# Kernel tuning notes

Hardware: AMD Instinct MI355X
Metric: run time of the kernel (lower is better)

Reference implementation:

```python
import jax, jax.numpy as jnp
import numpy as np

B = 4096          # number of graphs/segments
D = 256           # n_feature
O = 4             # n_output


def setup_inputs() -> dict:
    key = jax.random.key(0)
    k1, k2 = jax.random.split(key)
    # ragged segment sizes in [32, 96], concrete at trace time
    rng = np.random.default_rng(0)
    counts = rng.integers(32, 97, size=B).astype(np.int64)
    total = int(counts.sum())  # ~262144 nodes
    x = jax.random.normal(k1, (total, D), dtype=jnp.float32)
    W = jax.random.normal(k2, (O, D), dtype=jnp.float32) * (1.0 / np.sqrt(D))
    b = jnp.zeros((O,), dtype=jnp.float32)
    node_num = jnp.asarray(counts)
    return {"x": x, "node_num": node_num, "W": W, "b": b}


def reference(x, node_num, W, b):
    # x: [total_nodes, D]; node_num: [B] contiguous segment sizes
    total = x.shape[0]
    seg_ids = jnp.repeat(jnp.arange(B), node_num, total_repeat_length=total)
    seg_sum = jax.ops.segment_sum(x, seg_ids, num_segments=B)          # [B, D]
    mean = seg_sum / node_num[:, None].astype(x.dtype)                 # per-segment mean
    return jax.nn.sigmoid(mean @ W.T + b)                              # [B, O]
```

## Files before the change

kernel.cpp:

```cpp
#include <hip/hip_runtime.h>
#include <math.h>

#define SCAN_DIM 256

typedef float v4f __attribute__((ext_vector_type(4)));

__global__ void seg_offsets_kernel(const int* __restrict__ counts,
                                   int* __restrict__ offsets, int B) {
  __shared__ int partial[SCAN_DIM];
  const int tid = threadIdx.x;
  const int chunk = (B + SCAN_DIM - 1) / SCAN_DIM;
  const int base = tid * chunk;

  int s = 0;
  for (int i = 0; i < chunk; ++i) {
    const int idx = base + i;
    if (idx < B) s += counts[idx];
  }
  partial[tid] = s;
  __syncthreads();

  for (int off = 1; off < SCAN_DIM; off <<= 1) {
    int v = (tid >= off) ? partial[tid - off] : 0;
    __syncthreads();
    partial[tid] += v;
    __syncthreads();
  }

  int run = (tid == 0) ? 0 : partial[tid - 1];
  for (int i = 0; i < chunk; ++i) {
    const int idx = base + i;
    if (idx < B) {
      offsets[idx] = run;
      run += counts[idx];
    }
  }
}

__global__ __launch_bounds__(64) void mean_proj_kernel(
    const float* __restrict__ x, const int* __restrict__ counts,
    const int* __restrict__ offsets, const float* __restrict__ W,
    const float* __restrict__ b, float* __restrict__ out) {
  const int seg  = blockIdx.x;
  const int lane = threadIdx.x;

  const int  cnt   = counts[seg];
  const long start = (long)offsets[seg];

  const v4f* W4 = (const v4f*)W;
  const v4f w0 = W4[0 * 64 + lane];
  const v4f w1 = W4[1 * 64 + lane];
  const v4f w2 = W4[2 * 64 + lane];
  const v4f w3 = W4[3 * 64 + lane];

  float a0 = 0.f, a1 = 0.f, a2 = 0.f, a3 = 0.f;

  const v4f* p = (const v4f*)x + start * 64 + lane;

  int n = 0;
  v4f v0, v1, v2, v3;
  bool have = (3 < cnt);
  if (have) {
    v0 = __builtin_nontemporal_load(p + 0);
    v1 = __builtin_nontemporal_load(p + 64);
    v2 = __builtin_nontemporal_load(p + 128);
    v3 = __builtin_nontemporal_load(p + 192);
  }
  while (have) {
    const int nn = n + 4;
    const bool next = (nn + 3 < cnt);
    const v4f* q = p + 256;
    v4f u0, u1, u2, u3;
    if (next) {
      u0 = __builtin_nontemporal_load(q + 0);
      u1 = __builtin_nontemporal_load(q + 64);
      u2 = __builtin_nontemporal_load(q + 128);
      u3 = __builtin_nontemporal_load(q + 192);
    }

    a0 += v0.x * w0.x + v0.y * w0.y + v0.z * w0.z + v0.w * w0.w;
    a1 += v0.x * w1.x + v0.y * w1.y + v0.z * w1.z + v0.w * w1.w;
    a2 += v0.x * w2.x + v0.y * w2.y + v0.z * w2.z + v0.w * w2.w;
    a3 += v0.x * w3.x + v0.y * w3.y + v0.z * w3.z + v0.w * w3.w;

    a0 += v1.x * w0.x + v1.y * w0.y + v1.z * w0.z + v1.w * w0.w;
    a1 += v1.x * w1.x + v1.y * w1.y + v1.z * w1.z + v1.w * w1.w;
    a2 += v1.x * w2.x + v1.y * w2.y + v1.z * w2.z + v1.w * w2.w;
    a3 += v1.x * w3.x + v1.y * w3.y + v1.z * w3.z + v1.w * w3.w;

    a0 += v2.x * w0.x + v2.y * w0.y + v2.z * w0.z + v2.w * w0.w;
    a1 += v2.x * w1.x + v2.y * w1.y + v2.z * w1.z + v2.w * w1.w;
    a2 += v2.x * w2.x + v2.y * w2.y + v2.z * w2.z + v2.w * w2.w;
    a3 += v2.x * w3.x + v2.y * w3.y + v2.z * w3.z + v2.w * w3.w;

    a0 += v3.x * w0.x + v3.y * w0.y + v3.z * w0.z + v3.w * w0.w;
    a1 += v3.x * w1.x + v3.y * w1.y + v3.z * w1.z + v3.w * w1.w;
    a2 += v3.x * w2.x + v3.y * w2.y + v3.z * w2.z + v3.w * w2.w;
    a3 += v3.x * w3.x + v3.y * w3.y + v3.z * w3.z + v3.w * w3.w;

    if (next) { v0 = u0; v1 = u1; v2 = u2; v3 = u3; }
    p = q; n = nn; have = next;
  }
  {
    const v4f* t = (const v4f*)x + start * 64 + lane;
    for (; n < cnt; ++n) {
      const v4f v = __builtin_nontemporal_load(t + (long)n * 64);
      a0 += v.x * w0.x + v.y * w0.y + v.z * w0.z + v.w * w0.w;
      a1 += v.x * w1.x + v.y * w1.y + v.z * w1.z + v.w * w1.w;
      a2 += v.x * w2.x + v.y * w2.y + v.z * w2.z + v.w * w2.w;
      a3 += v.x * w3.x + v.y * w3.y + v.z * w3.z + v.w * w3.w;
    }
  }

  for (int off = 32; off > 0; off >>= 1) {
    a0 += __shfl_down(a0, off, 64);
    a1 += __shfl_down(a1, off, 64);
    a2 += __shfl_down(a2, off, 64);
    a3 += __shfl_down(a3, off, 64);
  }

  if (lane == 0) {
    const float inv = 1.0f / (float)cnt;
    v4f r;
    r.x = 1.0f / (1.0f + expf(-(a0 * inv + b[0])));
    r.y = 1.0f / (1.0f + expf(-(a1 * inv + b[1])));
    r.z = 1.0f / (1.0f + expf(-(a2 * inv + b[2])));
    r.w = 1.0f / (1.0f + expf(-(a3 * inv + b[3])));
    *(v4f*)(out + (long)seg * 4) = r;
  }
}

extern "C" void kernel_launch(void* const* d_in, const int* in_sizes, int n_in,
                              void* d_out, int out_size, void* d_ws, size_t ws_size,
                              hipStream_t stream) {
  const float* x        = (const float*)d_in[0];
  const int*   node_num = (const int*)d_in[1];
  const float* W        = (const float*)d_in[2];
  const float* b        = (const float*)d_in[3];
  float*       out      = (float*)d_out;

  const int B = in_sizes[1];
  int* offsets = (int*)d_ws;

  seg_offsets_kernel<<<1, SCAN_DIM, 0, stream>>>(node_num, offsets, B);
  mean_proj_kernel<<<B, 64, 0, stream>>>(x, node_num, offsets, W, b, out);
}
```

Measured before the change: 346.2 us.

## Balance work by splitting rows evenly across waves with atomic segment accumulation

Replaces one-wave-per-segment with a fixed grid of waves that each own an equal chunk of rows, locate their starting segment by binary search over offsets, and flush partial projections to a zeroed accumulator with atomics at segment boundaries. A third kernel then applies the mean scaling, bias and sigmoid. This targets load imbalance from ragged segment sizes and the short per-segment loops. In exchange it adds an extra launch, atomic traffic, per-row boundary checks, and a float summation order that is no longer deterministic.

```diff
diff --git a/kernel.cpp b/kernel.cpp
--- a/kernel.cpp
+++ b/kernel.cpp
@@ -2,11 +2,13 @@
 #include <math.h>
 
 #define SCAN_DIM 256
+#define NWAVES   4096
 
 typedef float v4f __attribute__((ext_vector_type(4)));
 
 __global__ void seg_offsets_kernel(const int* __restrict__ counts,
-                                   int* __restrict__ offsets, int B) {
+                                   int* __restrict__ offsets,
+                                   float* __restrict__ seg_acc, int B) {
   __shared__ int partial[SCAN_DIM];
   const int tid = threadIdx.x;
   const int chunk = (B + SCAN_DIM - 1) / SCAN_DIM;
@@ -35,17 +37,20 @@
       run += counts[idx];
     }
   }
+  if (tid == SCAN_DIM - 1) offsets[B] = run;
+
+  for (int i = tid; i < B * 4; i += SCAN_DIM) seg_acc[i] = 0.0f;
 }
 
-__global__ __launch_bounds__(64) void mean_proj_kernel(
-    const float* __restrict__ x, const int* __restrict__ counts,
-    const int* __restrict__ offsets, const float* __restrict__ W,
-    const float* __restrict__ b, float* __restrict__ out) {
-  const int seg  = blockIdx.x;
+__global__ __launch_bounds__(64) void proj_acc_kernel(
+    const float* __restrict__ x, const int* __restrict__ offsets,
+    const float* __restrict__ W, float* __restrict__ seg_acc,
+    int B, int T, int chunk) {
+  const int wave = blockIdx.x;
   const int lane = threadIdx.x;
-
-  const int  cnt   = counts[seg];
-  const long start = (long)offsets[seg];
+  const int r0 = wave * chunk;
+  if (r0 >= T) return;
+  const int r1 = min(r0 + chunk, T);
 
   const v4f* W4 = (const v4f*)W;
   const v4f w0 = W4[0 * 64 + lane];
@@ -53,13 +58,48 @@
   const v4f w2 = W4[2 * 64 + lane];
   const v4f w3 = W4[3 * 64 + lane];
 
+  int lo = 0, hi = B;
+  while (hi - lo > 1) {
+    const int mid = (lo + hi) >> 1;
+    if (offsets[mid] <= r0) lo = mid; else hi = mid;
+  }
+  int seg    = lo;
+  int segEnd = offsets[seg + 1];
+
   float a0 = 0.f, a1 = 0.f, a2 = 0.f, a3 = 0.f;
 
-  const v4f* p = (const v4f*)x + start * 64 + lane;
+  auto flush = [&]() {
+    float t0 = a0, t1 = a1, t2 = a2, t3 = a3;
+    for (int off = 32; off > 0; off >>= 1) {
+      t0 += __shfl_down(t0, off, 64);
+      t1 += __shfl_down(t1, off, 64);
+      t2 += __shfl_down(t2, off, 64);
+      t3 += __shfl_down(t3, off, 64);
+    }
+    if (lane == 0) {
+      atomicAdd(&seg_acc[seg * 4 + 0], t0);
+      atomicAdd(&seg_acc[seg * 4 + 1], t1);
+      atomicAdd(&seg_acc[seg * 4 + 2], t2);
+      atomicAdd(&seg_acc[seg * 4 + 3], t3);
+    }
+    a0 = a1 = a2 = a3 = 0.f;
+  };
 
-  int n = 0;
+#define ACC(v)                                                      \
+  a0 += (v).x * w0.x + (v).y * w0.y + (v).z * w0.z + (v).w * w0.w;  \
+  a1 += (v).x * w1.x + (v).y * w1.y + (v).z * w1.z + (v).w * w1.w;  \
+  a2 += (v).x * w2.x + (v).y * w2.y + (v).z * w2.z + (v).w * w2.w;  \
+  a3 += (v).x * w3.x + (v).y * w3.y + (v).z * w3.z + (v).w * w3.w;
+
+#define BOUNDARY(r)                                                 \
+  if ((r) == segEnd) { flush(); ++seg; segEnd = offsets[seg + 1]; }
+
+  const v4f* xb = (const v4f*)x + (long)r0 * 64 + lane;
+  const v4f* p  = xb;
+
+  int n = r0;
   v4f v0, v1, v2, v3;
-  bool have = (3 < cnt);
+  bool have = (n + 3 < r1);
   if (have) {
     v0 = __builtin_nontemporal_load(p + 0);
     v1 = __builtin_nontemporal_load(p + 64);
@@ -67,9 +107,9 @@
     v3 = __builtin_nontemporal_load(p + 192);
   }
   while (have) {
-    const int nn = n + 4;
-    const bool next = (nn + 3 < cnt);
-    const v4f* q = p + 256;
+    const int  nn   = n + 4;
+    const bool next = (nn + 3 < r1);
+    const v4f* q    = p + 256;
     v4f u0, u1, u2, u3;
     if (next) {
       u0 = __builtin_nontemporal_load(q + 0);
@@ -78,56 +118,39 @@
       u3 = __builtin_nontemporal_load(q + 192);
     }
 
-    a0 += v0.x * w0.x + v0.y * w0.y + v0.z * w0.z + v0.w * w0.w;
-    a1 += v0.x * w1.x + v0.y * w1.y + v0.z * w1.z + v0.w * w1.w;
-    a2 += v0.x * w2.x + v0.y * w2.y + v0.z * w2.z + v0.w * w2.w;
-    a3 += v0.x * w3.x + v0.y * w3.y + v0.z * w3.z + v0.w * w3.w;
-
-    a0 += v1.x * w0.x + v1.y * w0.y + v1.z * w0.z + v1.w * w0.w;
-    a1 += v1.x * w1.x + v1.y * w1.y + v1.z * w1.z + v1.w * w1.w;
-    a2 += v1.x * w2.x + v1.y * w2.y + v1.z * w2.z + v1.w * w2.w;
-    a3 += v1.x * w3.x + v1.y * w3.y + v1.z * w3.z + v1.w * w3.w;
-
-    a0 += v2.x * w0.x + v2.y * w0.y + v2.z * w0.z + v2.w * w0.w;
-    a1 += v2.x * w1.x + v2.y * w1.y + v2.z * w1.z + v2.w * w1.w;
-    a2 += v2.x * w2.x + v2.y * w2.y + v2.z * w2.z + v2.w * w2.w;
-    a3 += v2.x * w3.x + v2.y * w3.y + v2.z * w3.z + v2.w * w3.w;
-
-    a0 += v3.x * w0.x + v3.y * w0.y + v3.z * w0.z + v3.w * w0.w;
-    a1 += v3.x * w1.x + v3.y * w1.y + v3.z * w1.z + v3.w * w1.w;
-    a2 += v3.x * w2.x + v3.y * w2.y + v3.z * w2.z + v3.w * w2.w;
-    a3 += v3.x * w3.x + v3.y * w3.y + v3.z * w3.z + v3.w * w3.w;
+    BOUNDARY(n + 0) ACC(v0)
+    BOUNDARY(n + 1) ACC(v1)
+    BOUNDARY(n + 2) ACC(v2)
+    BOUNDARY(n + 3) ACC(v3)
 
     if (next) { v0 = u0; v1 = u1; v2 = u2; v3 = u3; }
     p = q; n = nn; have = next;
   }
-  {
-    const v4f* t = (const v4f*)x + start * 64 + lane;
-    for (; n < cnt; ++n) {
-      const v4f v = __builtin_nontemporal_load(t + (long)n * 64);
-      a0 += v.x * w0.x + v.y * w0.y + v.z * w0.z + v.w * w0.w;
-      a1 += v.x * w1.x + v.y * w1.y + v.z * w1.z + v.w * w1.w;
-      a2 += v.x * w2.x + v.y * w2.y + v.z * w2.z + v.w * w2.w;
-      a3 += v.x * w3.x + v.y * w3.y + v.z * w3.z + v.w * w3.w;
-    }
+  for (; n < r1; ++n) {
+    BOUNDARY(n)
+    const v4f v = __builtin_nontemporal_load(xb + (long)(n - r0) * 64);
+    ACC(v)
   }
+  flush();
 
-  for (int off = 32; off > 0; off >>= 1) {
-    a0 += __shfl_down(a0, off, 64);
-    a1 += __shfl_down(a1, off, 64);
-    a2 += __shfl_down(a2, off, 64);
-    a3 += __shfl_down(a3, off, 64);
-  }
+#undef ACC
+#undef BOUNDARY
+}
 
-  if (lane == 0) {
-    const float inv = 1.0f / (float)cnt;
-    v4f r;
-    r.x = 1.0f / (1.0f + expf(-(a0 * inv + b[0])));
-    r.y = 1.0f / (1.0f + expf(-(a1 * inv + b[1])));
-    r.z = 1.0f / (1.0f + expf(-(a2 * inv + b[2])));
-    r.w = 1.0f / (1.0f + expf(-(a3 * inv + b[3])));
-    *(v4f*)(out + (long)seg * 4) = r;
-  }
+__global__ void finish_kernel(const float* __restrict__ seg_acc,
+                              const int* __restrict__ counts,
+                              const float* __restrict__ b,
+                              float* __restrict__ out, int B) {
+  const int i = blockIdx.x * blockDim.x + threadIdx.x;
+  if (i >= B) return;
+  const v4f acc = ((const v4f*)seg_acc)[i];
+  const float inv = 1.0f / (float)counts[i];
+  v4f r;
+  r.x = 1.0f / (1.0f + expf(-(acc.x * inv + b[0])));
+  r.y = 1.0f / (1.0f + expf(-(acc.y * inv + b[1])));
+  r.z = 1.0f / (1.0f + expf(-(acc.z * inv + b[2])));
+  r.w = 1.0f / (1.0f + expf(-(acc.w * inv + b[3])));
+  ((v4f*)out)[i] = r;
 }
 
 extern "C" void kernel_launch(void* const* d_in, const int* in_sizes, int n_in,
@@ -140,8 +163,13 @@
   float*       out      = (float*)d_out;
 
   const int B = in_sizes[1];
-  int* offsets = (int*)d_ws;
+  const int T = in_sizes[0] / 256;
+  const int chunk = (T + NWAVES - 1) / NWAVES;
 
-  seg_offsets_kernel<<<1, SCAN_DIM, 0, stream>>>(node_num, offsets, B);
-  mean_proj_kernel<<<B, 64, 0, stream>>>(x, node_num, offsets, W, b, out);
+  int*   offsets = (int*)d_ws;
+  float* seg_acc = (float*)((char*)d_ws + 32768);
+
+  seg_offsets_kernel<<<1, SCAN_DIM, 0, stream>>>(node_num, offsets, seg_acc, B);
+  proj_acc_kernel<<<NWAVES, 64, 0, stream>>>(x, offsets, W, seg_acc, B, T, chunk);
+  finish_kernel<<<(B + 255) / 256, 256, 0, stream>>>(seg_acc, node_num, b, out, B);
 }
```

Measured after the change: 351.9 us. Within noise of the previous version (+1.7%).
